# Performance work log

Hardware: AMD Instinct MI355X
Metric: run time of the kernel (lower is better)

The kernel has to match this reference:

```python
import jax, jax.numpy as jnp
import numpy as np

L, E, S, H, D, V = 6, 384, 256, 6, 64, 65
FF = 4 * E


def _ln(x, g, b, ddof, eps=1e-5):
    mean = jnp.mean(x, axis=-1, keepdims=True)
    var = jnp.var(x, axis=-1, keepdims=True, ddof=ddof)
    return g * (x - mean) / jnp.sqrt(var + eps) + b


def setup_inputs() -> dict:
    key = jax.random.key(0)
    ks = jax.random.split(key, 16)
    std = 0.02
    inp = {
        'x': jax.random.randint(ks[0], (64, S), 0, V),
        'tok_emb': jax.random.normal(ks[1], (V, E)) * std,
        'pos_emb': jax.random.normal(ks[2], (S, E)) * std,
        'Wq': jax.random.normal(ks[3], (L, E, H * D)) * std,
        'Wk': jax.random.normal(ks[4], (L, E, H * D)) * std,
        'Wv': jax.random.normal(ks[5], (L, E, H * D)) * std,
        'Wproj': jax.random.normal(ks[6], (L, H * D, E)) * std,
        'bproj': jnp.zeros((L, E)),
        'W1': jax.random.normal(ks[7], (L, E, FF)) * std,
        'b1': jnp.zeros((L, FF)),
        'W2': jax.random.normal(ks[8], (L, FF, E)) * std,
        'b2': jnp.zeros((L, E)),
        'ln1_g': jnp.ones((L, E)), 'ln1_b': jnp.zeros((L, E)),
        'ln2_g': jnp.ones((L, E)), 'ln2_b': jnp.zeros((L, E)),
        'lnf_g': jnp.ones((E,)), 'lnf_b': jnp.zeros((E,)),
        'Wlm': jax.random.normal(ks[9], (E, V)) * std,
        'blm': jnp.zeros((V,)),
    }
    return inp


def _forward(x, tok_emb, pos_emb, Wq, Wk, Wv, Wproj, bproj, W1, b1, W2, b2,
             ln1_g, ln1_b, ln2_g, ln2_b, lnf_g, lnf_b, Wlm, blm):
    B, T = x.shape
    h = tok_emb[x] + pos_emb[:T]  # [B,T,E]
    causal = jnp.tril(jnp.ones((T, T), dtype=bool))
    neg_inf = jnp.finfo(h.dtype).min
    for l in range(L):
        hn = _ln(h, ln1_g[l], ln1_b[l], ddof=1)  # custom LayerNorm uses unbiased var
        q = (hn @ Wq[l]).reshape(B, T, H, D)
        k = (hn @ Wk[l]).reshape(B, T, H, D)
        v = (hn @ Wv[l]).reshape(B, T, H, D)
        wei = jnp.einsum('bqhd,bkhd->bhqk', q, k) * (D ** -0.5)
        wei = jnp.where(causal, wei, neg_inf)
        wei = jax.nn.softmax(wei, axis=-1)
        att = jnp.einsum('bhqk,bkhd->bqhd', wei, v).reshape(B, T, H * D)
        h = h + att @ Wproj[l] + bproj[l]
        hn = _ln(h, ln2_g[l], ln2_b[l], ddof=1)
        h = h + jax.nn.relu(hn @ W1[l] + b1[l]) @ W2[l] + b2[l]
    h = _ln(h, lnf_g, lnf_b, ddof=0)  # nn.LayerNorm uses biased var
    return h @ Wlm + blm  # logits [B,T,V]


def reference(x, tok_emb, pos_emb, Wq, Wk, Wv, Wproj, bproj, W1, b1, W2, b2,
              ln1_g, ln1_b, ln2_g, ln2_b, lnf_g, lnf_b, Wlm, blm):
    return _forward(x, tok_emb, pos_emb, Wq, Wk, Wv, Wproj, bproj, W1, b1, W2, b2,
                    ln1_g, ln1_b, ln2_g, ln2_b, lnf_g, lnf_b, Wlm, blm)
```

## Files before the change

kernel.cpp:

```cpp
#include <hip/hip_runtime.h>

#define L_  6
#define E_  384
#define T_  256
#define H_  6
#define D_  64
#define V_  65
#define FF_ 1536
#define B_  64
#define BT_ (B_*T_)
#define HD_ 384

typedef __attribute__((ext_vector_type(8))) short short8;
typedef __attribute__((ext_vector_type(4))) float f32x4;
typedef unsigned short us;
typedef unsigned int u32;

__device__ __forceinline__ us f2bf(float f) {
  u32 u = __float_as_uint(f);
  u32 r = (u + 0x7fffu + ((u >> 16) & 1u)) >> 16;
  return (us)r;
}
__device__ __forceinline__ float bf2f(us v) {
  return __uint_as_float(((u32)v) << 16);
}

__device__ __forceinline__ int xcd_swz(int b, int nwg) {
  const int q = nwg >> 3;
  return (b & 7) * q + (b >> 3);
}

__global__ void embed_kernel(const int* __restrict__ x, const float* __restrict__ tok,
                             const float* __restrict__ pos, us* __restrict__ h) {
  const int total8 = BT_ * E_ / 8;
  for (int i = blockIdx.x * blockDim.x + threadIdx.x; i < total8;
       i += gridDim.x * blockDim.x) {
    const int flat = i << 3;
    const int row  = flat / E_;
    const int e    = flat - row * E_;
    const int id   = x[row];
    const float4 a0 = *reinterpret_cast<const float4*>(tok + id * E_ + e);
    const float4 a1 = *reinterpret_cast<const float4*>(tok + id * E_ + e + 4);
    const float4 p0 = *reinterpret_cast<const float4*>(pos + (row & (T_ - 1)) * E_ + e);
    const float4 p1 = *reinterpret_cast<const float4*>(pos + (row & (T_ - 1)) * E_ + e + 4);
    short8 o;
    o[0] = (short)f2bf(a0.x + p0.x); o[1] = (short)f2bf(a0.y + p0.y);
    o[2] = (short)f2bf(a0.z + p0.z); o[3] = (short)f2bf(a0.w + p0.w);
    o[4] = (short)f2bf(a1.x + p1.x); o[5] = (short)f2bf(a1.y + p1.y);
    o[6] = (short)f2bf(a1.z + p1.z); o[7] = (short)f2bf(a1.w + p1.w);
    *reinterpret_cast<short8*>(h + flat) = o;
  }
}

template<int DDOF>
__global__ void stats_kernel(const us* __restrict__ h, float2* __restrict__ st) {
  const int wave = threadIdx.x >> 6;
  const int lane = threadIdx.x & 63;
  const int row  = (blockIdx.x << 2) + wave;
  float sum = 0.f, sq = 0.f;
  if (lane < 48) {
    const short8 v = *reinterpret_cast<const short8*>(h + (size_t)row * E_ + lane * 8);
#pragma unroll
    for (int j = 0; j < 8; ++j) {
      const float f = bf2f((us)v[j]);
      sum += f; sq += f * f;
    }
  }
#pragma unroll
  for (int off = 32; off > 0; off >>= 1) {
    sum += __shfl_xor(sum, off);
    sq  += __shfl_xor(sq, off);
  }
  if (lane == 0) {
    const float mean = sum * (1.f / E_);
    const float var  = (sq - E_ * mean * mean) * (1.f / (E_ - DDOF));
    float2 o; o.x = mean; o.y = rsqrtf(var + 1e-5f);
    st[row] = o;
  }
}

__global__ void transpose_w(const float* __restrict__ src, us* __restrict__ dst,
                            int K, int N, int Ndst, long srcLS, long dstLS,
                            const float* __restrict__ g) {
  __shared__ float t[32][33];
  const int n0 = blockIdx.x << 5, k0 = blockIdx.y << 5;
  const int tx = threadIdx.x & 31, ty = threadIdx.x >> 5;
  const float* s = src + (size_t)blockIdx.z * srcLS;
  us* d = dst + (size_t)blockIdx.z * dstLS;
#pragma unroll
  for (int j = 0; j < 32; j += 8) {
    const int n = n0 + tx;
    t[ty + j][tx] = (n < N) ? s[(size_t)(k0 + ty + j) * N + n] : 0.f;
  }
  __syncthreads();
  const float gk = g ? g[blockIdx.z * 384 + k0 + tx] : 1.f;
#pragma unroll
  for (int j = 0; j < 32; j += 8) {
    const int n = n0 + ty + j;
    if (n < Ndst) d[(size_t)n * K + k0 + tx] = f2bf(t[tx][ty + j] * gk);
  }
}

__global__ void c12_kernel(const float* __restrict__ W, const float* __restrict__ g,
                           const float* __restrict__ b, float2* __restrict__ out,
                           int N, long srcLS, int outLS) {
  __shared__ float p1[4][64], p2[4][64];
  const int t = threadIdx.x;
  const int c = t & 63, kq = t >> 6;
  const int n = (blockIdx.x << 6) + c;
  const float* Wz = W + (size_t)blockIdx.y * srcLS;
  const float* gz = g + blockIdx.y * 384;
  const float* bz = b + blockIdx.y * 384;
  float s1 = 0.f, s2 = 0.f;
  if (n < N) {
    for (int k = kq * 96; k < kq * 96 + 96; ++k) {
      const float w = Wz[(size_t)k * N + n];
      s1 = fmaf(gz[k], w, s1);
      s2 = fmaf(bz[k], w, s2);
    }
  }
  p1[kq][c] = s1; p2[kq][c] = s2;
  __syncthreads();
  if (t < 64) {
    const int nn = (blockIdx.x << 6) + t;
    if (nn < N) {
      float2 o;
      o.x = p1[0][t] + p1[1][t] + p1[2][t] + p1[3][t];
      o.y = p2[0][t] + p2[1][t] + p2[2][t] + p2[3][t];
      out[(size_t)blockIdx.y * outLS + nn] = o;
    }
  }
}

template<int ROWS, int CHPR, int NTH>
__device__ __forceinline__ void stageG(const us* g, int rowUs, us* lds, int tid) {
#pragma unroll
  for (int j = 0; j < ROWS * CHPR / NTH; ++j) {
    const int fl  = j * NTH + tid;
    const int row = fl / CHPR;
    const int c   = fl % CHPR;
    const int gc  = (CHPR == 8) ? (c ^ (row & 7)) : (c ^ ((row >> 1) & 3));
    const us* src = g + (size_t)row * rowUs + gc * 8;
    __builtin_amdgcn_global_load_lds(
        (const __attribute__((address_space(1))) u32*)src,
        (__attribute__((address_space(3))) u32*)(lds + ((fl >> 6) << 9)),
        16, 0, 0);
  }
}

#define GEMM_LOOP(K_, NT_)                                                        \
  const int NT = (NT_);                                                           \
  _Pragma("unroll")                                                               \
  for (int p = 0; p < BUFS - 1; ++p) {                                            \
    stageG<BM, 4, 256>(Abase + p * 32, (K_), As[p], tid);                         \
    stageG<BN, 4, 256>(Bbase + p * 32, (K_), Bs[p], tid);                         \
  }                                                                               \
  int cb = 0;                                                                     \
  for (int t = 0; t < NT; ++t) {                                                  \
    if constexpr (BUFS == 4) {                                                    \
      if (t < NT - 2)       asm volatile("s_waitcnt vmcnt(%0)" :: "n"(2 * LPS) : "memory"); \
      else if (t == NT - 2) asm volatile("s_waitcnt vmcnt(%0)" :: "n"(LPS) : "memory");     \
      else                  asm volatile("s_waitcnt vmcnt(0)" ::: "memory");      \
    } else {                                                                      \
      if (t < NT - 1)       asm volatile("s_waitcnt vmcnt(%0)" :: "n"(LPS) : "memory");     \
      else                  asm volatile("s_waitcnt vmcnt(0)" ::: "memory");      \
    }                                                                             \
    __builtin_amdgcn_s_barrier();                                                 \
    __builtin_amdgcn_sched_barrier(0);                                            \
    if (t + BUFS - 1 < NT) {                                                      \
      int ib = cb + (BUFS - 1); if (ib >= BUFS) ib -= BUFS;                       \
      stageG<BM, 4, 256>(Abase + (t + BUFS - 1) * 32, (K_), As[ib], tid);         \
      stageG<BN, 4, 256>(Bbase + (t + BUFS - 1) * 32, (K_), Bs[ib], tid);         \
    }                                                                             \
    short8 af[FM], bfr[FN];                                                       \
    _Pragma("unroll")                                                             \
    for (int mt = 0; mt < FM; ++mt) {                                             \
      const int row = wm + mt * 16 + fm;                                          \
      af[mt] = *(const short8*)(As[cb] + row * 32 + ((fg ^ ((row >> 1) & 3)) << 3)); \
    }                                                                             \
    _Pragma("unroll")                                                             \
    for (int nt = 0; nt < FN; ++nt) {                                             \
      const int row = wn + nt * 16 + fm;                                          \
      bfr[nt] = *(const short8*)(Bs[cb] + row * 32 + ((fg ^ ((row >> 1) & 3)) << 3)); \
    }                                                                             \
    _Pragma("unroll")                                                             \
    for (int mt = 0; mt < FM; ++mt)                                               \
      _Pragma("unroll")                                                           \
      for (int nt = 0; nt < FN; ++nt)                                             \
        acc[mt][nt] = __builtin_amdgcn_mfma_f32_16x16x32_bf16(af[mt], bfr[nt], acc[mt][nt], 0, 0, 0); \
    cb = (cb + 1 == BUFS) ? 0 : cb + 1;                                           \
  }

template<int FM, int FN, int BUFS>
__global__ __launch_bounds__(256)
void gemm_mfma(const us* __restrict__ A, const us* __restrict__ Bt,
               const float* __restrict__ bias, const us* Res,
               us* __restrict__ O, int N, int K, int gx) {
  constexpr int BM = FM * 32, BN = FN * 32;
  constexpr int LPS = (BM + BN) * 4 / 256;
  __shared__ us As[BUFS][BM * 32];
  __shared__ us Bs[BUFS][BN * 32];
  const int tid = threadIdx.x;
  const int lid = xcd_swz(blockIdx.x, gridDim.x);
  const int bnI = lid % gx, bmI = lid / gx;
  const int bm = bmI * BM, bn = bnI * BN;
  const int wv = tid >> 6, ln = tid & 63;
  const int fm = ln & 15, fg = ln >> 4;
  const int wm = (wv >> 1) * (FM * 16), wn = (wv & 1) * (FN * 16);
  const us* Abase = A + (size_t)bm * K;
  const us* Bbase = Bt + (size_t)bn * K;

  f32x4 acc[FM][FN];
  const f32x4 zz = {0.f, 0.f, 0.f, 0.f};
#pragma unroll
  for (int i = 0; i < FM; ++i)
#pragma unroll
    for (int j = 0; j < FN; ++j) acc[i][j] = zz;

  GEMM_LOOP(K, K >> 5)

#pragma unroll
  for (int mt = 0; mt < FM; ++mt) {
#pragma unroll
    for (int nt = 0; nt < FN; ++nt) {
      const int col  = bn + wn + nt * 16 + fm;
      const int row0 = bm + wm + mt * 16 + fg * 4;
      const float bc = bias[col];
#pragma unroll
      for (int r = 0; r < 4; ++r) {
        const size_t idx = (size_t)(row0 + r) * N + col;
        O[idx] = f2bf(acc[mt][nt][r] + bc + bf2f(Res[idx]));
      }
    }
  }
}

template<int FM, int FN, int EPI, int BUFS>
__global__ __launch_bounds__(256)
void gemm_fold(const us* __restrict__ A, const us* __restrict__ Bt,
               const float2* __restrict__ st, const float2* __restrict__ c12,
               const float* __restrict__ bias, void* O0, void* O1,
               int N, int gx) {
  constexpr int K = 384;
  constexpr int BM = FM * 32, BN = FN * 32;
  constexpr int LPS = (BM + BN) * 4 / 256;
  __shared__ us As[BUFS][BM * 32];
  __shared__ us Bs[BUFS][BN * 32];
  const int tid = threadIdx.x;
  const int lid = xcd_swz(blockIdx.x, gridDim.x);
  const int bnI = lid % gx, bmI = lid / gx;
  const int bm = bmI * BM, bn = bnI * BN;
  const int wv = tid >> 6, ln = tid & 63;
  const int fm = ln & 15, fg = ln >> 4;
  const int wm = (wv >> 1) * (FM * 16), wn = (wv & 1) * (FN * 16);
  const us* Abase = A + (size_t)bm * K;
  const us* Bbase = Bt + (size_t)bn * K;

  f32x4 acc[FM][FN];
  const f32x4 zz = {0.f, 0.f, 0.f, 0.f};
#pragma unroll
  for (int i = 0; i < FM; ++i)
#pragma unroll
    for (int j = 0; j < FN; ++j) acc[i][j] = zz;

  GEMM_LOOP(K, 12)

#pragma unroll
  for (int mt = 0; mt < FM; ++mt) {
    const int row0 = bm + wm + mt * 16 + fg * 4;
    float2 sr[4];
#pragma unroll
    for (int r = 0; r < 4; ++r) sr[r] = st[row0 + r];
#pragma unroll
    for (int nt = 0; nt < FN; ++nt) {
      const int col = bn + wn + nt * 16 + fm;
      if (EPI == 3 && col >= V_) continue;
      const float2 cc = c12[col];
      float vals[4];
#pragma unroll
      for (int r = 0; r < 4; ++r)
        vals[r] = sr[r].y * (acc[mt][nt][r] - sr[r].x * cc.x) + cc.y;
      if (EPI == 0) {
        if (col < 768) {
          us* qk = (us*)O0;
#pragma unroll
          for (int r = 0; r < 4; ++r)
            qk[(size_t)(row0 + r) * 768 + col] = f2bf(vals[r]);
        } else {
          const int d = col - 768;
          const int hh = d >> 6, dd = d & 63;
          const int bI = row0 >> 8, t0 = row0 & 255;
          us* vt = (us*)O1;
          ushort4 pk;
          pk.x = f2bf(vals[0]); pk.y = f2bf(vals[1]);
          pk.z = f2bf(vals[2]); pk.w = f2bf(vals[3]);
          *reinterpret_cast<ushort4*>(vt + ((size_t)((bI * H_ + hh) * 64 + dd)) * 256 + t0) = pk;
        }
      } else if (EPI == 2) {
        us* o = (us*)O0;
        const float bc = bias[col];
#pragma unroll
        for (int r = 0; r < 4; ++r)
          o[(size_t)(row0 + r) * N + col] = f2bf(fmaxf(vals[r] + bc, 0.f));
      } else {
        float* o = (float*)O0;
        const float bc = bias[col];
#pragma unroll
        for (int r = 0; r < 4; ++r)
          o[(size_t)(row0 + r) * V_ + col] = vals[r] + bc;
      }
    }
  }
}

__global__ __launch_bounds__(256)
void attn_mfma(const us* __restrict__ qk, const us* __restrict__ vT,
               us* __restrict__ ab) {
  __shared__ us Ks[2][64 * 64];
  __shared__ us Vs[2][64 * 64];
  __shared__ us Plds[4][16 * 72];
  const int tid = threadIdx.x, w = tid >> 6, l = tid & 63;
  const int m = l & 15, g = l >> 4;
  const int bi = xcd_swz(blockIdx.x, gridDim.x);
  const int b = bi / 24, rem = bi - b * 24, h = rem >> 2, qt = rem & 3;
  const int qrow = (b << 8) + (qt << 6) + (w << 4);
  const us* Kg = qk + (size_t)(b << 8) * 768 + 384 + h * 64;
  const us* Vg = vT + (size_t)(b * H_ + h) * 64 * 256;

  short8 qf0, qf1;
  {
    const us* qp = qk + (size_t)(qrow + m) * 768 + h * 64 + g * 8;
    qf0 = *(const short8*)qp;
    qf1 = *(const short8*)(qp + 32);
  }
  float mrow[4], ssum[4];
  f32x4 o[4];
  const f32x4 zz = {0.f, 0.f, 0.f, 0.f};
#pragma unroll
  for (int r = 0; r < 4; ++r) { mrow[r] = -1e30f; ssum[r] = 0.f; o[r] = zz; }

  stageG<64, 8, 256>(Kg, 768, Ks[0], tid);
  stageG<64, 8, 256>(Vg, 256, Vs[0], tid);
  __syncthreads();

  int cur = 0;
  for (int kt = 0; kt <= qt; ++kt) {
    if (kt < qt) {
      stageG<64, 8, 256>(Kg + (size_t)(kt + 1) * 64 * 768, 768, Ks[cur ^ 1], tid);
      stageG<64, 8, 256>(Vg + (kt + 1) * 64,               256, Vs[cur ^ 1], tid);
    }
    f32x4 s[4];
#pragma unroll
    for (int nt = 0; nt < 4; ++nt) {
      const int row = nt * 16 + m;
      const int sw  = row & 7;
      short8 kf0 = *(const short8*)(Ks[cur] + row * 64 + ((g ^ sw) << 3));
      short8 kf1 = *(const short8*)(Ks[cur] + row * 64 + (((4 | g) ^ sw) << 3));
      f32x4 z = zz;
      z = __builtin_amdgcn_mfma_f32_16x16x32_bf16(qf0, kf0, z, 0, 0, 0);
      z = __builtin_amdgcn_mfma_f32_16x16x32_bf16(qf1, kf1, z, 0, 0, 0);
      s[nt] = z;
    }
    const bool diag = (kt == qt);
    float p[4][4], tmax[4];
#pragma unroll
    for (int r = 0; r < 4; ++r) tmax[r] = -1e30f;
#pragma unroll
    for (int nt = 0; nt < 4; ++nt)
#pragma unroll
      for (int r = 0; r < 4; ++r) {
        float v = s[nt][r] * 0.125f;
        if (diag) {
          const int key = nt * 16 + m;
          const int qq  = (w << 4) + (g << 2) + r;
          if (key > qq) v = -1e30f;
        }
        p[nt][r] = v;
        tmax[r] = fmaxf(tmax[r], v);
      }
#pragma unroll
    for (int xm = 1; xm < 16; xm <<= 1)
#pragma unroll
      for (int r = 0; r < 4; ++r) tmax[r] = fmaxf(tmax[r], __shfl_xor(tmax[r], xm));
    float sc[4], tsum[4];
#pragma unroll
    for (int r = 0; r < 4; ++r) {
      const float nm = fmaxf(mrow[r], tmax[r]);
      sc[r] = __expf(mrow[r] - nm);
      mrow[r] = nm;
      tsum[r] = 0.f;
    }
#pragma unroll
    for (int nt = 0; nt < 4; ++nt)
#pragma unroll
      for (int r = 0; r < 4; ++r) {
        p[nt][r] = __expf(p[nt][r] - mrow[r]);
        tsum[r] += p[nt][r];
      }
#pragma unroll
    for (int xm = 1; xm < 16; xm <<= 1)
#pragma unroll
      for (int r = 0; r < 4; ++r) tsum[r] += __shfl_xor(tsum[r], xm);
#pragma unroll
    for (int r = 0; r < 4; ++r) ssum[r] = ssum[r] * sc[r] + tsum[r];
#pragma unroll
    for (int nt = 0; nt < 4; ++nt)
#pragma unroll
      for (int r = 0; r < 4; ++r) o[nt][r] *= sc[r];
#pragma unroll
    for (int nt = 0; nt < 4; ++nt)
#pragma unroll
      for (int r = 0; r < 4; ++r)
        Plds[w][(g * 4 + r) * 72 + nt * 16 + m] = f2bf(p[nt][r]);
#pragma unroll
    for (int kc = 0; kc < 2; ++kc) {
      short8 pa = *(const short8*)&Plds[w][m * 72 + kc * 32 + g * 8];
#pragma unroll
      for (int nd = 0; nd < 4; ++nd) {
        const int row = nd * 16 + m;
        short8 vf = *(const short8*)(Vs[cur] + row * 64 + ((((kc << 2) | g) ^ (row & 7)) << 3));
        o[nd] = __builtin_amdgcn_mfma_f32_16x16x32_bf16(pa, vf, o[nd], 0, 0, 0);
      }
    }
    __syncthreads();
    cur ^= 1;
  }
#pragma unroll
  for (int r = 0; r < 4; ++r) {
    const float inv = 1.f / ssum[r];
    const size_t rowoff = (size_t)(qrow + g * 4 + r) * 384 + h * 64;
#pragma unroll
    for (int nd = 0; nd < 4; ++nd)
      ab[rowoff + nd * 16 + m] = f2bf(o[nd][r] * inv);
  }
}

extern "C" void kernel_launch(void* const* d_in, const int* in_sizes, int n_in,
                              void* d_out, int out_size, void* d_ws, size_t ws_size,
                              hipStream_t stream) {
  const int*   x    = (const int*)  d_in[0];
  const float* tok  = (const float*)d_in[1];
  const float* pos  = (const float*)d_in[2];
  const float* Wq   = (const float*)d_in[3];
  const float* Wk   = (const float*)d_in[4];
  const float* Wv   = (const float*)d_in[5];
  const float* Wpr  = (const float*)d_in[6];
  const float* bpr  = (const float*)d_in[7];
  const float* W1   = (const float*)d_in[8];
  const float* b1   = (const float*)d_in[9];
  const float* W2   = (const float*)d_in[10];
  const float* b2   = (const float*)d_in[11];
  const float* ln1g = (const float*)d_in[12];
  const float* ln1b = (const float*)d_in[13];
  const float* ln2g = (const float*)d_in[14];
  const float* ln2b = (const float*)d_in[15];
  const float* lnfg = (const float*)d_in[16];
  const float* lnfb = (const float*)d_in[17];
  const float* Wlm  = (const float*)d_in[18];
  const float* blm  = (const float*)d_in[19];
  float* out = (float*)d_out;

  char* W = (char*)d_ws;
  us*     h    = (us*)(W + 0);
  us*     qkb  = (us*)(W + 12582912);
  us*     vTb  = (us*)(W + 37748736);
  us*     abb  = (us*)(W + 50331648);
  us*     ffa  = (us*)(W + 12582912);
  us*     qkvT = (us*)(W + 62914560);
  us*     projT= (us*)(W + 68222976);
  us*     W1T  = (us*)(W + 69992448);
  us*     W2T  = (us*)(W + 77070336);
  us*     WlmT = (us*)(W + 84148224);
  float2* st   = (float2*)(W + 84246528);
  float2* c12q = (float2*)(W + 84377600);
  float2* c12f = (float2*)(W + 84432896);
  float2* c12lm= (float2*)(W + 84506624);

  transpose_w<<<dim3(12,12,6), 256, 0, stream>>>(Wq,  qkvT,           384, 384, 384, 147456, 442368, ln1g);
  transpose_w<<<dim3(12,12,6), 256, 0, stream>>>(Wk,  qkvT + 147456,  384, 384, 384, 147456, 442368, ln1g);
  transpose_w<<<dim3(12,12,6), 256, 0, stream>>>(Wv,  qkvT + 294912,  384, 384, 384, 147456, 442368, ln1g);
  transpose_w<<<dim3(12,12,6), 256, 0, stream>>>(Wpr, projT,          384, 384, 384, 147456, 147456, nullptr);
  transpose_w<<<dim3(48,12,6), 256, 0, stream>>>(W1,  W1T,            384, 1536, 1536, 589824, 589824, ln2g);
  transpose_w<<<dim3(12,48,6), 256, 0, stream>>>(W2,  W2T,            1536, 384, 384, 589824, 589824, nullptr);
  transpose_w<<<dim3(4,12,1),  256, 0, stream>>>(Wlm, WlmT,           384, 65, 128, 0, 0, lnfg);

  c12_kernel<<<dim3(6,6),  256, 0, stream>>>(Wq,  ln1g, ln1b, c12q,       384, 147456, 1152);
  c12_kernel<<<dim3(6,6),  256, 0, stream>>>(Wk,  ln1g, ln1b, c12q + 384, 384, 147456, 1152);
  c12_kernel<<<dim3(6,6),  256, 0, stream>>>(Wv,  ln1g, ln1b, c12q + 768, 384, 147456, 1152);
  c12_kernel<<<dim3(24,6), 256, 0, stream>>>(W1,  ln2g, ln2b, c12f,       1536, 589824, 1536);
  c12_kernel<<<dim3(2,1),  256, 0, stream>>>(Wlm, lnfg, lnfb, c12lm,      65, 0, 0);

  embed_kernel<<<3072, 256, 0, stream>>>(x, tok, pos, h);

  for (int l = 0; l < L_; ++l) {
    stats_kernel<1><<<BT_/4, 256, 0, stream>>>(h, st);
    gemm_fold<4,4,0,3><<<1152, 256, 0, stream>>>(
        h, qkvT + (size_t)l*442368, st, c12q + (size_t)l*1152, nullptr,
        qkb, vTb, 1152, 9);
    attn_mfma<<<B_*H_*4, 256, 0, stream>>>(qkb, vTb, abb);
    gemm_mfma<2,4,4><<<768, 256, 0, stream>>>(
        abb, projT + (size_t)l*147456, bpr + l*E_, h, h, 384, 384, 3);
    stats_kernel<1><<<BT_/4, 256, 0, stream>>>(h, st);
    gemm_fold<4,4,2,3><<<1536, 256, 0, stream>>>(
        h, W1T + (size_t)l*589824, st, c12f + (size_t)l*1536, b1 + l*FF_,
        ffa, nullptr, 1536, 12);
    gemm_mfma<2,4,4><<<768, 256, 0, stream>>>(
        ffa, W2T + (size_t)l*589824, b2 + l*E_, h, h, 384, 1536, 3);
  }

  stats_kernel<0><<<BT_/4, 256, 0, stream>>>(h, st);
  gemm_fold<2,4,3,3><<<256, 256, 0, stream>>>(
      h, WlmT, st, c12lm, blm, out, nullptr, 128, 1);
}
```

Baseline: 966.8 us.

## Fuse LayerNorm row statistics into residual GEMM epilogues via atomics

Removes the per-layer stats kernels by having the residual-writing GEMM epilogues compute per-row sum and sum-of-squares of the rounded bf16 outputs. These are reduced across lanes and atomically added into per-stage buffers, which are zeroed once with a memset at the start. The consuming fold GEMMs now derive mean and inverse std from the raw sums. This saves 12 kernel launches and the extra passes over h, at the cost of atomic traffic, a larger workspace and a memset.

```diff
diff --git a/kernel.cpp b/kernel.cpp
--- a/kernel.cpp
+++ b/kernel.cpp
@@ -52,8 +52,7 @@
   }
 }
 
-template<int DDOF>
-__global__ void stats_kernel(const us* __restrict__ h, float2* __restrict__ st) {
+__global__ void stats_kernel(const us* __restrict__ h, float* __restrict__ st) {
   const int wave = threadIdx.x >> 6;
   const int lane = threadIdx.x & 63;
   const int row  = (blockIdx.x << 2) + wave;
@@ -72,10 +71,8 @@
     sq  += __shfl_xor(sq, off);
   }
   if (lane == 0) {
-    const float mean = sum * (1.f / E_);
-    const float var  = (sq - E_ * mean * mean) * (1.f / (E_ - DDOF));
-    float2 o; o.x = mean; o.y = rsqrtf(var + 1e-5f);
-    st[row] = o;
+    st[row * 2]     = sum;
+    st[row * 2 + 1] = sq;
   }
 }
 
@@ -195,7 +192,8 @@
 __global__ __launch_bounds__(256)
 void gemm_mfma(const us* __restrict__ A, const us* __restrict__ Bt,
                const float* __restrict__ bias, const us* Res,
-               us* __restrict__ O, int N, int K, int gx) {
+               us* __restrict__ O, float* __restrict__ stA,
+               int N, int K, int gx) {
   constexpr int BM = FM * 32, BN = FN * 32;
   constexpr int LPS = (BM + BN) * 4 / 256;
   __shared__ us As[BUFS][BM * 32];
@@ -219,6 +217,12 @@
 
   GEMM_LOOP(K, K >> 5)
 
+  float rs[FM][4], rq[FM][4];
+#pragma unroll
+  for (int mt = 0; mt < FM; ++mt)
+#pragma unroll
+    for (int r = 0; r < 4; ++r) { rs[mt][r] = 0.f; rq[mt][r] = 0.f; }
+
 #pragma unroll
   for (int mt = 0; mt < FM; ++mt) {
 #pragma unroll
@@ -229,16 +233,41 @@
 #pragma unroll
       for (int r = 0; r < 4; ++r) {
         const size_t idx = (size_t)(row0 + r) * N + col;
-        O[idx] = f2bf(acc[mt][nt][r] + bc + bf2f(Res[idx]));
-      }
-    }
-  }
-}
-
-template<int FM, int FN, int EPI, int BUFS>
+        const float v = acc[mt][nt][r] + bc + bf2f(Res[idx]);
+        const float vb = bf2f(f2bf(v));
+        O[idx] = f2bf(v);
+        rs[mt][r] += vb;
+        rq[mt][r] = fmaf(vb, vb, rq[mt][r]);
+      }
+    }
+  }
+#pragma unroll
+  for (int off = 1; off < 16; off <<= 1) {
+#pragma unroll
+    for (int mt = 0; mt < FM; ++mt)
+#pragma unroll
+      for (int r = 0; r < 4; ++r) {
+        rs[mt][r] += __shfl_xor(rs[mt][r], off);
+        rq[mt][r] += __shfl_xor(rq[mt][r], off);
+      }
+  }
+  if (fm == 0) {
+#pragma unroll
+    for (int mt = 0; mt < FM; ++mt) {
+      const int row0 = bm + wm + mt * 16 + fg * 4;
+#pragma unroll
+      for (int r = 0; r < 4; ++r) {
+        atomicAdd(stA + (row0 + r) * 2,     rs[mt][r]);
+        atomicAdd(stA + (row0 + r) * 2 + 1, rq[mt][r]);
+      }
+    }
+  }
+}
+
+template<int FM, int FN, int EPI, int BUFS, int DDOF>
 __global__ __launch_bounds__(256)
 void gemm_fold(const us* __restrict__ A, const us* __restrict__ Bt,
-               const float2* __restrict__ st, const float2* __restrict__ c12,
+               const float* __restrict__ st, const float2* __restrict__ c12,
                const float* __restrict__ bias, void* O0, void* O1,
                int N, int gx) {
   constexpr int K = 384;
@@ -268,9 +297,15 @@
 #pragma unroll
   for (int mt = 0; mt < FM; ++mt) {
     const int row0 = bm + wm + mt * 16 + fg * 4;
-    float2 sr[4];
-#pragma unroll
-    for (int r = 0; r < 4; ++r) sr[r] = st[row0 + r];
+    float mu[4], iv[4];
+#pragma unroll
+    for (int r = 0; r < 4; ++r) {
+      const float sum = st[(row0 + r) * 2];
+      const float sq  = st[(row0 + r) * 2 + 1];
+      mu[r] = sum * (1.f / 384.f);
+      const float var = (sq - 384.f * mu[r] * mu[r]) * (1.f / (384 - DDOF));
+      iv[r] = rsqrtf(var + 1e-5f);
+    }
 #pragma unroll
     for (int nt = 0; nt < FN; ++nt) {
       const int col = bn + wn + nt * 16 + fm;
@@ -279,7 +314,7 @@
       float vals[4];
 #pragma unroll
       for (int r = 0; r < 4; ++r)
-        vals[r] = sr[r].y * (acc[mt][nt][r] - sr[r].x * cc.x) + cc.y;
+        vals[r] = iv[r] * (acc[mt][nt][r] - mu[r] * cc.x) + cc.y;
       if (EPI == 0) {
         if (col < 768) {
           us* qk = (us*)O0;
@@ -471,10 +506,12 @@
   us*     W1T  = (us*)(W + 69992448);
   us*     W2T  = (us*)(W + 77070336);
   us*     WlmT = (us*)(W + 84148224);
-  float2* st   = (float2*)(W + 84246528);
-  float2* c12q = (float2*)(W + 84377600);
-  float2* c12f = (float2*)(W + 84432896);
-  float2* c12lm= (float2*)(W + 84506624);
+  float*  stAcc= (float*)(W + 84246528);
+  float2* c12q = (float2*)(W + 85950464);
+  float2* c12f = (float2*)(W + 86005760);
+  float2* c12lm= (float2*)(W + 86079488);
+
+  hipMemsetAsync(stAcc, 0, 13 * BT_ * 2 * sizeof(float), stream);
 
   transpose_w<<<dim3(12,12,6), 256, 0, stream>>>(Wq,  qkvT,           384, 384, 384, 147456, 442368, ln1g);
   transpose_w<<<dim3(12,12,6), 256, 0, stream>>>(Wk,  qkvT + 147456,  384, 384, 384, 147456, 442368, ln1g);
@@ -491,24 +528,24 @@
   c12_kernel<<<dim3(2,1),  256, 0, stream>>>(Wlm, lnfg, lnfb, c12lm,      65, 0, 0);
 
   embed_kernel<<<3072, 256, 0, stream>>>(x, tok, pos, h);
+  stats_kernel<<<BT_/4, 256, 0, stream>>>(h, stAcc);
 
   for (int l = 0; l < L_; ++l) {
-    stats_kernel<1><<<BT_/4, 256, 0, stream>>>(h, st);
-    gemm_fold<4,4,0,3><<<1152, 256, 0, stream>>>(
-        h, qkvT + (size_t)l*442368, st, c12q + (size_t)l*1152, nullptr,
-        qkb, vTb, 1152, 9);
+    gemm_fold<4,4,0,3,1><<<1152, 256, 0, stream>>>(
+        h, qkvT + (size_t)l*442368, stAcc + (size_t)(2*l)*BT_*2,
+        c12q + (size_t)l*1152, nullptr, qkb, vTb, 1152, 9);
     attn_mfma<<<B_*H_*4, 256, 0, stream>>>(qkb, vTb, abb);
     gemm_mfma<2,4,4><<<768, 256, 0, stream>>>(
-        abb, projT + (size_t)l*147456, bpr + l*E_, h, h, 384, 384, 3);
-    stats_kernel<1><<<BT_/4, 256, 0, stream>>>(h, st);
-    gemm_fold<4,4,2,3><<<1536, 256, 0, stream>>>(
-        h, W1T + (size_t)l*589824, st, c12f + (size_t)l*1536, b1 + l*FF_,
-        ffa, nullptr, 1536, 12);
+        abb, projT + (size_t)l*147456, bpr + l*E_, h, h,
+        stAcc + (size_t)(2*l+1)*BT_*2, 384, 384, 3);
+    gemm_fold<4,4,2,3,1><<<1536, 256, 0, stream>>>(
+        h, W1T + (size_t)l*589824, stAcc + (size_t)(2*l+1)*BT_*2,
+        c12f + (size_t)l*1536, b1 + l*FF_, ffa, nullptr, 1536, 12);
     gemm_mfma<2,4,4><<<768, 256, 0, stream>>>(
-        ffa, W2T + (size_t)l*589824, b2 + l*E_, h, h, 384, 1536, 3);
-  }
-
-  stats_kernel<0><<<BT_/4, 256, 0, stream>>>(h, st);
-  gemm_fold<2,4,3,3><<<256, 256, 0, stream>>>(
-      h, WlmT, st, c12lm, blm, out, nullptr, 128, 1);
-}
+        ffa, W2T + (size_t)l*589824, b2 + l*E_, h, h,
+        stAcc + (size_t)(2*l+2)*BT_*2, 384, 1536, 3);
+  }
+
+  gemm_fold<2,4,3,3,0><<<256, 256, 0, stream>>>(
+      h, WlmT, stAcc + (size_t)12*BT_*2, c12lm, blm, out, nullptr, 128, 1);
+}
```

After: 1.045 ms. 8.0% more time.

## Merge QKV weight prep kernels and shrink LN-folded GEMM tiles

Applied to the files above, without the earlier changes.

Folds the three Q/K/V weight transposes and the three c12 reductions into single launches, one each, which cuts per-forward launch overhead. The LayerNorm-folded GEMMs for QKV, FFN1 and the LM head get new template parameters: the M tile shrinks and the fourth parameter changes, so QKV and FFN1 launch twice as many blocks. The smaller tiles are meant to raise parallelism and occupancy, at the cost of less weight reuse per block.

```diff
diff --git a/kernel.cpp b/kernel.cpp
--- a/kernel.cpp
+++ b/kernel.cpp
@@ -101,6 +101,25 @@
   }
 }
 
+__global__ void transpose_qkv(const float* __restrict__ Wq, const float* __restrict__ Wk,
+                              const float* __restrict__ Wv, us* __restrict__ dst,
+                              const float* __restrict__ g) {
+  __shared__ float t[32][33];
+  const int sel = blockIdx.z / 6, l = blockIdx.z % 6;
+  const float* s = (sel == 0 ? Wq : sel == 1 ? Wk : Wv) + (size_t)l * 147456;
+  us* d = dst + (size_t)l * 442368 + sel * 147456;
+  const int n0 = blockIdx.x << 5, k0 = blockIdx.y << 5;
+  const int tx = threadIdx.x & 31, ty = threadIdx.x >> 5;
+#pragma unroll
+  for (int j = 0; j < 32; j += 8)
+    t[ty + j][tx] = s[(size_t)(k0 + ty + j) * 384 + n0 + tx];
+  __syncthreads();
+  const float gk = g[l * 384 + k0 + tx];
+#pragma unroll
+  for (int j = 0; j < 32; j += 8)
+    d[(size_t)(n0 + ty + j) * 384 + k0 + tx] = f2bf(t[tx][ty + j] * gk);
+}
+
 __global__ void c12_kernel(const float* __restrict__ W, const float* __restrict__ g,
                            const float* __restrict__ b, float2* __restrict__ out,
                            int N, long srcLS, int outLS) {
@@ -129,6 +148,34 @@
       o.y = p2[0][t] + p2[1][t] + p2[2][t] + p2[3][t];
       out[(size_t)blockIdx.y * outLS + nn] = o;
     }
+  }
+}
+
+__global__ void c12_qkv(const float* __restrict__ Wq, const float* __restrict__ Wk,
+                        const float* __restrict__ Wv, const float* __restrict__ g,
+                        const float* __restrict__ b, float2* __restrict__ out) {
+  __shared__ float p1[4][64], p2[4][64];
+  const int sel = blockIdx.y / 6, l = blockIdx.y % 6;
+  const float* Wz = (sel == 0 ? Wq : sel == 1 ? Wk : Wv) + (size_t)l * 147456;
+  const float* gz = g + l * 384;
+  const float* bz = b + l * 384;
+  const int t = threadIdx.x;
+  const int c = t & 63, kq = t >> 6;
+  const int n = (blockIdx.x << 6) + c;
+  float s1 = 0.f, s2 = 0.f;
+  for (int k = kq * 96; k < kq * 96 + 96; ++k) {
+    const float w = Wz[(size_t)k * 384 + n];
+    s1 = fmaf(gz[k], w, s1);
+    s2 = fmaf(bz[k], w, s2);
+  }
+  p1[kq][c] = s1; p2[kq][c] = s2;
+  __syncthreads();
+  if (t < 64) {
+    const int nn = (blockIdx.x << 6) + t;
+    float2 o;
+    o.x = p1[0][t] + p1[1][t] + p1[2][t] + p1[3][t];
+    o.y = p2[0][t] + p2[1][t] + p2[2][t] + p2[3][t];
+    out[(size_t)l * 1152 + sel * 384 + nn] = o;
   }
 }
 
@@ -476,32 +523,28 @@
   float2* c12f = (float2*)(W + 84432896);
   float2* c12lm= (float2*)(W + 84506624);
 
-  transpose_w<<<dim3(12,12,6), 256, 0, stream>>>(Wq,  qkvT,           384, 384, 384, 147456, 442368, ln1g);
-  transpose_w<<<dim3(12,12,6), 256, 0, stream>>>(Wk,  qkvT + 147456,  384, 384, 384, 147456, 442368, ln1g);
-  transpose_w<<<dim3(12,12,6), 256, 0, stream>>>(Wv,  qkvT + 294912,  384, 384, 384, 147456, 442368, ln1g);
-  transpose_w<<<dim3(12,12,6), 256, 0, stream>>>(Wpr, projT,          384, 384, 384, 147456, 147456, nullptr);
-  transpose_w<<<dim3(48,12,6), 256, 0, stream>>>(W1,  W1T,            384, 1536, 1536, 589824, 589824, ln2g);
-  transpose_w<<<dim3(12,48,6), 256, 0, stream>>>(W2,  W2T,            1536, 384, 384, 589824, 589824, nullptr);
-  transpose_w<<<dim3(4,12,1),  256, 0, stream>>>(Wlm, WlmT,           384, 65, 128, 0, 0, lnfg);
-
-  c12_kernel<<<dim3(6,6),  256, 0, stream>>>(Wq,  ln1g, ln1b, c12q,       384, 147456, 1152);
-  c12_kernel<<<dim3(6,6),  256, 0, stream>>>(Wk,  ln1g, ln1b, c12q + 384, 384, 147456, 1152);
-  c12_kernel<<<dim3(6,6),  256, 0, stream>>>(Wv,  ln1g, ln1b, c12q + 768, 384, 147456, 1152);
-  c12_kernel<<<dim3(24,6), 256, 0, stream>>>(W1,  ln2g, ln2b, c12f,       1536, 589824, 1536);
-  c12_kernel<<<dim3(2,1),  256, 0, stream>>>(Wlm, lnfg, lnfb, c12lm,      65, 0, 0);
+  transpose_qkv<<<dim3(12,12,18), 256, 0, stream>>>(Wq, Wk, Wv, qkvT, ln1g);
+  transpose_w<<<dim3(12,12,6), 256, 0, stream>>>(Wpr, projT, 384, 384, 384, 147456, 147456, nullptr);
+  transpose_w<<<dim3(48,12,6), 256, 0, stream>>>(W1,  W1T,   384, 1536, 1536, 589824, 589824, ln2g);
+  transpose_w<<<dim3(12,48,6), 256, 0, stream>>>(W2,  W2T,   1536, 384, 384, 589824, 589824, nullptr);
+  transpose_w<<<dim3(4,12,1),  256, 0, stream>>>(Wlm, WlmT,  384, 65, 128, 0, 0, lnfg);
+
+  c12_qkv<<<dim3(6,18), 256, 0, stream>>>(Wq, Wk, Wv, ln1g, ln1b, c12q);
+  c12_kernel<<<dim3(24,6), 256, 0, stream>>>(W1,  ln2g, ln2b, c12f,  1536, 589824, 1536);
+  c12_kernel<<<dim3(2,1),  256, 0, stream>>>(Wlm, lnfg, lnfb, c12lm, 65, 0, 0);
 
   embed_kernel<<<3072, 256, 0, stream>>>(x, tok, pos, h);
 
   for (int l = 0; l < L_; ++l) {
     stats_kernel<1><<<BT_/4, 256, 0, stream>>>(h, st);
-    gemm_fold<4,4,0,3><<<1152, 256, 0, stream>>>(
+    gemm_fold<2,4,0,4><<<2304, 256, 0, stream>>>(
         h, qkvT + (size_t)l*442368, st, c12q + (size_t)l*1152, nullptr,
         qkb, vTb, 1152, 9);
     attn_mfma<<<B_*H_*4, 256, 0, stream>>>(qkb, vTb, abb);
     gemm_mfma<2,4,4><<<768, 256, 0, stream>>>(
         abb, projT + (size_t)l*147456, bpr + l*E_, h, h, 384, 384, 3);
     stats_kernel<1><<<BT_/4, 256, 0, stream>>>(h, st);
-    gemm_fold<4,4,2,3><<<1536, 256, 0, stream>>>(
+    gemm_fold<2,4,2,4><<<3072, 256, 0, stream>>>(
         h, W1T + (size_t)l*589824, st, c12f + (size_t)l*1536, b1 + l*FF_,
         ffa, nullptr, 1536, 12);
     gemm_mfma<2,4,4><<<768, 256, 0, stream>>>(
@@ -509,6 +552,6 @@
   }
 
   stats_kernel<0><<<BT_/4, 256, 0, stream>>>(h, st);
-  gemm_fold<2,4,3,3><<<256, 256, 0, stream>>>(
+  gemm_fold<2,4,3,4><<<256, 256, 0, stream>>>(
       h, WlmT, st, c12lm, blm, out, nullptr, 128, 1);
 }
```

Measured after the change: 1.015 ms. 1.05x slower.
